# Optimization experiments

Hardware: AMD Instinct MI355X
Metric: run time of the kernel (lower is better)

The kernel has to match this reference:

```python
import jax, jax.numpy as jnp
import numpy as np

ALPHA = 0.2  # leaky relu slope
NEG_BIG = -9000000000000000.0


def setup_inputs() -> dict:
    key = jax.random.key(0)
    k1, k2, k3, k4 = jax.random.split(key, 4)
    B, N, Fin, Fout = 8, 2048, 256, 256
    h = jax.random.normal(k1, (B, N, Fin), dtype=jnp.float32)
    adj = jax.random.randint(k2, (B, N, N), 0, 2, dtype=jnp.int32)
    # xavier_uniform with gain=1.414
    gain = 1.414
    limW = gain * np.sqrt(6.0 / (Fin + Fout))
    W = jax.random.uniform(k3, (Fin, Fout), dtype=jnp.float32, minval=-limW, maxval=limW)
    lima = gain * np.sqrt(6.0 / (2 * Fout + 1))
    a = jax.random.uniform(k4, (2 * Fout, 1), dtype=jnp.float32, minval=-lima, maxval=lima)
    return {"h": h, "adj": adj, "W": W, "a": a}


def reference(h, adj, W, a):
    # Wh: [B, N, F]
    Wh = jnp.matmul(h, W)
    Fout = W.shape[1]
    a1 = a[:Fout, 0]   # scores for source node i (repeat_interleave side)
    a2 = a[Fout:, 0]   # scores for target node j (repeat side)
    # e[b,i,j] = leakyrelu(Wh[b,i]@a1 + Wh[b,j]@a2)  -- decomposed, no O(N^2 * 2F) tensor
    s1 = jnp.einsum('bnf,f->bn', Wh, a1)  # [B, N]
    s2 = jnp.einsum('bnf,f->bn', Wh, a2)  # [B, N]
    e = jax.nn.leaky_relu(s1[:, :, None] + s2[:, None, :], negative_slope=ALPHA)
    masked = jnp.where(adj > 0, e, jnp.full_like(e, NEG_BIG))
    attention = jax.nn.softmax(masked, axis=2)  # dropout=0 (eval mode)
    h_prime = jnp.matmul(attention, Wh)  # [B, N, F]
    return jax.nn.elu(h_prime)
```

## Files before the change

### kernel.cpp

```cpp
#include <hip/hip_runtime.h>

typedef __attribute__((ext_vector_type(8))) short bhalf8;
typedef __attribute__((ext_vector_type(4))) float floatx4;

#define ALPHA_LR 0.2f

__device__ __forceinline__ unsigned short f2bf(float f) {
  union { float f; unsigned int u; } v; v.f = f;
  unsigned int r = v.u + 0x7fffu + ((v.u >> 16) & 1u);
  return (unsigned short)(r >> 16);
}
__device__ __forceinline__ float bf2f(unsigned short u) {
  union { unsigned int u; float f; } v; v.u = ((unsigned int)u) << 16;
  return v.f;
}
__device__ __forceinline__ void gld16(const void* g, void* l) {
  __builtin_amdgcn_global_load_lds((const __attribute__((address_space(1))) unsigned int*)g,
                                   (__attribute__((address_space(3))) unsigned int*)l,
                                   16, 0, 0);
}

__global__ void k0w_split(const float* __restrict__ W,
                          unsigned short* __restrict__ WThi,
                          unsigned short* __restrict__ WTlo,
                          unsigned int* __restrict__ s2maxEnc) {
  __shared__ float s[16][17];
  const int tx = threadIdx.x, ty = threadIdx.y;
  if (blockIdx.x == 0 && blockIdx.y == 0 && ty == 0 && tx < 8) s2maxEnc[tx] = 0u;
  const int n0 = blockIdx.x * 16, k0 = blockIdx.y * 16;
  s[ty][tx] = W[(k0 + ty) * 256 + n0 + tx];
  __syncthreads();
  float v = s[tx][ty];
  const int k = k0 + tx, n = n0 + ty;
  unsigned short hi = f2bf(v);
  unsigned short lo = f2bf(v - bf2f(hi));
  const int idx = (k >> 5) * 8192 + n * 32 + (k & 31);
  WThi[idx] = hi;
  WTlo[idx] = lo;
}

__global__ __launch_bounds__(256) void k2_pack(const int* __restrict__ adj,
                                               unsigned long long* __restrict__ mask) {
  const int wave = threadIdx.x >> 6, lane = threadIdx.x & 63;
  const long wid = (long)blockIdx.x * 4 + wave;
  const long u0 = wid * 64;
  const int* base = adj + u0 * 64 + lane;
#pragma unroll
  for (int it = 0; it < 64; it += 4) {
    int v0 = base[(it + 0) * 64];
    int v1 = base[(it + 1) * 64];
    int v2 = base[(it + 2) * 64];
    int v3 = base[(it + 3) * 64];
    unsigned long long m0 = __ballot(v0 > 0);
    unsigned long long m1 = __ballot(v1 > 0);
    unsigned long long m2 = __ballot(v2 > 0);
    unsigned long long m3 = __ballot(v3 > 0);
    if (lane == 0) {
      mask[u0 + it + 0] = m0;
      mask[u0 + it + 1] = m1;
      mask[u0 + it + 2] = m2;
      mask[u0 + it + 3] = m3;
    }
  }
}

__global__ __launch_bounds__(512, 2) void k1_mfma(const float* __restrict__ h,
                                                  const unsigned short* __restrict__ Bhi_g,
                                                  const unsigned short* __restrict__ Blo_g,
                                                  const float* __restrict__ a_g,
                                                  unsigned short* __restrict__ WhPack,
                                                  float* __restrict__ s1,
                                                  float* __restrict__ s2,
                                                  unsigned int* __restrict__ s2maxEnc) {
  __shared__ unsigned short Ah[64 * 264], Al[64 * 264];
  __shared__ unsigned short Bh[2][8192], Bl[2][8192];
  __shared__ float s1red[64], s2red[64];
  const int t = threadIdx.x;
  const long r0 = (long)blockIdx.x * 64;
  const int wave = t >> 6, lane = t & 63;

  if (t < 64) { s1red[t] = 0.f; s2red[t] = 0.f; }

#pragma unroll
  for (int rep = 0; rep < 2; rep++) {
    const int off = wave * 1024 + rep * 512;
    gld16(Bhi_g + off + lane * 8, &Bh[0][off]);
    gld16(Blo_g + off + lane * 8, &Bl[0][off]);
  }

#pragma unroll
  for (int q = 0; q < 8; q++) {
    int idx = q * 512 + t;
    int row = idx >> 6, c4 = idx & 63;
    float4 x = *(const float4*)(h + (r0 + row) * 256 + c4 * 4);
    float xs[4] = {x.x, x.y, x.z, x.w};
    unsigned short hs[4], ls[4];
#pragma unroll
    for (int qq = 0; qq < 4; qq++) {
      hs[qq] = f2bf(xs[qq]);
      ls[qq] = f2bf(xs[qq] - bf2f(hs[qq]));
    }
    *(ushort4*)&Ah[row * 264 + c4 * 4] = (ushort4){hs[0], hs[1], hs[2], hs[3]};
    *(ushort4*)&Al[row * 264 + c4 * 4] = (ushort4){ls[0], ls[1], ls[2], ls[3]};
  }
  __syncthreads();

  const int wm = wave >> 2, wn = wave & 3;
  const int lhi = lane >> 4, llo = lane & 15;

  floatx4 acc[2][4];
#pragma unroll
  for (int mt = 0; mt < 2; mt++)
#pragma unroll
    for (int nt = 0; nt < 4; nt++) acc[mt][nt] = (floatx4){0.f, 0.f, 0.f, 0.f};

  for (int ks = 0; ks < 8; ks++) {
    const int cur = ks & 1, nxt = cur ^ 1, ksn = (ks + 1) & 7;
#pragma unroll
    for (int rep = 0; rep < 2; rep++) {
      const int off = wave * 1024 + rep * 512;
      gld16(Bhi_g + ksn * 8192 + off + lane * 8, &Bh[nxt][off]);
      gld16(Blo_g + ksn * 8192 + off + lane * 8, &Bl[nxt][off]);
    }

    const int k0 = ks * 32;
    bhalf8 ah[2], al[2], bh[4], bl[4];
#pragma unroll
    for (int mt = 0; mt < 2; mt++) {
      int ro = (wm * 32 + mt * 16 + llo) * 264 + k0 + lhi * 8;
      ah[mt] = *(const bhalf8*)&Ah[ro];
      al[mt] = *(const bhalf8*)&Al[ro];
    }
#pragma unroll
    for (int nt = 0; nt < 4; nt++) {
      int ro = (wn * 64 + nt * 16 + llo) * 32 + lhi * 8;
      bh[nt] = *(const bhalf8*)&Bh[cur][ro];
      bl[nt] = *(const bhalf8*)&Bl[cur][ro];
    }
#pragma unroll
    for (int mt = 0; mt < 2; mt++)
#pragma unroll
      for (int nt = 0; nt < 4; nt++) {
        acc[mt][nt] = __builtin_amdgcn_mfma_f32_16x16x32_bf16(ah[mt], bh[nt], acc[mt][nt], 0, 0, 0);
        acc[mt][nt] = __builtin_amdgcn_mfma_f32_16x16x32_bf16(ah[mt], bl[nt], acc[mt][nt], 0, 0, 0);
        acc[mt][nt] = __builtin_amdgcn_mfma_f32_16x16x32_bf16(al[mt], bh[nt], acc[mt][nt], 0, 0, 0);
      }
    __syncthreads();
  }

  float a1v[4], a2v[4];
#pragma unroll
  for (int nt = 0; nt < 4; nt++) {
    int f = wn * 64 + nt * 16 + llo;
    a1v[nt] = a_g[f];
    a2v[nt] = a_g[256 + f];
  }

  const int b = (int)(r0 >> 11);
  const int jt_base = (int)((r0 & 2047) >> 5);

#pragma unroll
  for (int mt = 0; mt < 2; mt++) {
    float p1[4], p2[4];
#pragma unroll
    for (int reg = 0; reg < 4; reg++) {
      p1[reg] = acc[mt][0][reg] * a1v[0] + acc[mt][1][reg] * a1v[1] +
                acc[mt][2][reg] * a1v[2] + acc[mt][3][reg] * a1v[3];
      p2[reg] = acc[mt][0][reg] * a2v[0] + acc[mt][1][reg] * a2v[1] +
                acc[mt][2][reg] * a2v[2] + acc[mt][3][reg] * a2v[3];
    }
#pragma unroll
    for (int off = 1; off < 16; off <<= 1) {
#pragma unroll
      for (int reg = 0; reg < 4; reg++) {
        p1[reg] += __shfl_xor(p1[reg], off);
        p2[reg] += __shfl_xor(p2[reg], off);
      }
    }
    if (llo == 0) {
#pragma unroll
      for (int reg = 0; reg < 4; reg++) {
        int il = wm * 32 + mt * 16 + lhi * 4 + reg;
        atomicAdd(&s1red[il], p1[reg]);
        atomicAdd(&s2red[il], p2[reg]);
      }
    }
#pragma unroll
    for (int nt = 0; nt < 4; nt++) {
      int f = wn * 64 + nt * 16 + llo;
      int jt = jt_base + wm;
      ushort4 pk = (ushort4){f2bf(acc[mt][nt][0]), f2bf(acc[mt][nt][1]),
                             f2bf(acc[mt][nt][2]), f2bf(acc[mt][nt][3])};
      *(ushort4*)&WhPack[((long)((b * 64 + jt) * 256 + f)) * 32 + mt * 16 + lhi * 4] = pk;
    }
  }

  __syncthreads();
  if (t < 64) {
    s1[r0 + t] = s1red[t];
    s2[r0 + t] = s2red[t];
    float v = s2red[t];
#pragma unroll
    for (int o = 32; o; o >>= 1) v = fmaxf(v, __shfl_xor(v, o));
    if (t == 0) {
      unsigned int u = __float_as_uint(v);
      unsigned int key = (u & 0x80000000u) ? ~u : (u | 0x80000000u);
      atomicMax(s2maxEnc + b, key);
    }
  }
}

__global__ __launch_bounds__(512, 2) void k3_attn(const unsigned short* __restrict__ WhPack,
                                                  const unsigned int* __restrict__ mask32,
                                                  const float* __restrict__ s1g,
                                                  const float* __restrict__ s2g,
                                                  const unsigned int* __restrict__ s2maxEnc,
                                                  float* __restrict__ out) {
  const int t = threadIdx.x;
  const int lin = blockIdx.x;
  const int b = lin & 7;
  const int ig = lin >> 3;
  const int wave = t >> 6, lane = t & 63;
  const int rg = wave >> 2, fg = wave & 3;
  const int i0 = ig * 64 + rg * 32;
  const long gr0 = (long)b * 2048 + i0;
  const int llo = lane & 15, lhi = lane >> 4;
  const int sh = lhi * 8;

  const unsigned int ek = s2maxEnc[b];
  const float s2max = (ek & 0x80000000u) ? __uint_as_float(ek & 0x7fffffffu)
                                         : __uint_as_float(~ek);
  float s1i[2], Mi[2];
#pragma unroll
  for (int mt = 0; mt < 2; mt++) {
    s1i[mt] = s1g[gr0 + mt * 16 + llo];
    float xm = s1i[mt] + s2max;
    Mi[mt] = fmaxf(xm, ALPHA_LR * xm);
  }

  const float* s2p = s2g + (long)b * 2048 + lhi * 8;
  const unsigned int* mp0 = mask32 + (gr0 + llo) * 64;
  const unsigned int* mp1 = mp0 + 16 * 64;
  const unsigned short* wb =
      WhPack + (long)b * 524288 + (long)((fg * 64 + llo) * 32 + lhi * 8);

  unsigned int cm0 = mp0[0], cm1 = mp1[0];
  float4 s2A = *(const float4*)s2p;
  float4 s2B = *(const float4*)(s2p + 4);
  bhalf8 bF[4];
#pragma unroll
  for (int nt = 0; nt < 4; nt++) bF[nt] = *(const bhalf8*)(wb + nt * 512);

  floatx4 acc[2][4];
#pragma unroll
  for (int mt = 0; mt < 2; mt++)
#pragma unroll
    for (int nt = 0; nt < 4; nt++) acc[mt][nt] = (floatx4){0.f, 0.f, 0.f, 0.f};
  float ls0 = 0.f, ls1 = 0.f;

#pragma unroll 2
  for (int jt = 0; jt < 64; jt++) {
    const int jn = (jt < 63) ? jt + 1 : 63;

    bhalf8 bFn[4];
#pragma unroll
    for (int nt = 0; nt < 4; nt++)
      bFn[nt] = *(const bhalf8*)(wb + (long)jn * 8192 + nt * 512);
    float4 s2nA = *(const float4*)(s2p + jn * 32);
    float4 s2nB = *(const float4*)(s2p + jn * 32 + 4);
    unsigned int nm0 = mp0[jn], nm1 = mp1[jn];

    __builtin_amdgcn_sched_barrier(0);

    bhalf8 pa[2];
#pragma unroll
    for (int mt = 0; mt < 2; mt++) {
      const float s1v = s1i[mt], miv = Mi[mt];
      const unsigned int mb = ((mt ? cm1 : cm0) >> sh) & 0xffu;
      float xs[8] = {s2A.x, s2A.y, s2A.z, s2A.w, s2B.x, s2B.y, s2B.z, s2B.w};
      float e[8];
      float lsm = 0.f;
#pragma unroll
      for (int q = 0; q < 8; q++) {
        float x = s1v + xs[q];
        float lk = fmaxf(x, ALPHA_LR * x);
        float ee = __expf(lk - miv);
        ee = (mb & (1u << q)) ? ee : 0.f;
        lsm += ee;
        e[q] = ee;
      }
      if (mt) ls1 += lsm; else ls0 += lsm;
      union { unsigned int u[4]; bhalf8 v; } pk;
#pragma unroll
      for (int q = 0; q < 4; q++)
        asm("v_cvt_pk_bf16_f32 %0, %1, %2" : "=v"(pk.u[q]) : "v"(e[2 * q]), "v"(e[2 * q + 1]));
      pa[mt] = pk.v;
    }

#pragma unroll
    for (int mt = 0; mt < 2; mt++)
#pragma unroll
      for (int nt = 0; nt < 4; nt++)
        acc[mt][nt] = __builtin_amdgcn_mfma_f32_16x16x32_bf16(mt ? pa[1] : pa[0],
                                                              bF[nt], acc[mt][nt], 0, 0, 0);

    cm0 = nm0; cm1 = nm1;
    s2A = s2nA; s2B = s2nB;
#pragma unroll
    for (int nt = 0; nt < 4; nt++) bF[nt] = bFn[nt];
  }

  ls0 += __shfl_xor(ls0, 16); ls0 += __shfl_xor(ls0, 32);
  ls1 += __shfl_xor(ls1, 16); ls1 += __shfl_xor(ls1, 32);
  float inv0 = 1.f / fmaxf(ls0, 1e-35f);
  float inv1 = 1.f / fmaxf(ls1, 1e-35f);

#pragma unroll
  for (int mt = 0; mt < 2; mt++) {
#pragma unroll
    for (int reg = 0; reg < 4; reg++) {
      const int rloc = lhi * 4 + reg;
      float iv = __shfl(mt ? inv1 : inv0, rloc);
      const long orow = (gr0 + mt * 16 + rloc) * 256 + fg * 64 + llo;
#pragma unroll
      for (int nt = 0; nt < 4; nt++) {
        float v = acc[mt][nt][reg] * iv;
        v = v > 0.f ? v : expm1f(v);
        out[orow + nt * 16] = v;
      }
    }
  }
}

extern "C" void kernel_launch(void* const* d_in, const int* in_sizes, int n_in,
                              void* d_out, int out_size, void* d_ws, size_t ws_size,
                              hipStream_t stream) {
  const float* h = (const float*)d_in[0];
  const int* adj = (const int*)d_in[1];
  const float* W = (const float*)d_in[2];
  const float* a = (const float*)d_in[3];
  float* out = (float*)d_out;

  char* ws = (char*)d_ws;
  unsigned short* WhPack = (unsigned short*)ws;
  unsigned short* WThi = (unsigned short*)(ws + 8388608);
  unsigned short* WTlo = (unsigned short*)(ws + 8519680);
  float* s1 = (float*)(ws + 8650752);
  float* s2 = (float*)(ws + 8716288);
  unsigned int* s2maxEnc = (unsigned int*)(ws + 8781824);
  unsigned long long* adjMask = (unsigned long long*)(ws + 8912896);

  hipLaunchKernelGGL(k0w_split, dim3(16, 16), dim3(16, 16), 0, stream, W, WThi, WTlo, s2maxEnc);
  hipLaunchKernelGGL(k1_mfma, dim3(256), dim3(512), 0, stream, h, WThi, WTlo, a,
                     WhPack, s1, s2, s2maxEnc);
  hipLaunchKernelGGL(k2_pack, dim3(2048), dim3(256), 0, stream, adj, adjMask);
  hipLaunchKernelGGL(k3_attn, dim3(256), dim3(512), 0, stream, WhPack,
                     (const unsigned int*)adjMask, s1, s2, s2maxEnc, out);
}
```

Measured before the change: 297.1 us.

## Compute attention probabilities once per block via shared-memory tile, double-buffered

The attention kernel now uses 32-row blocks of 256 threads, launched as twice as many blocks. Each thread computes the exp scores for 4 columns of one row and writes them as bf16 into a double-buffered shared-memory P tile. Each wave then reads its MFMA A operand from that tile and covers 128 output features with 8 accumulators. This removes the redundant per-wave recomputation of exps across feature groups, at the cost of an LDS barrier every iteration and more registers per thread. Wh B-fragments are no longer prefetched a step ahead, and the row sums are reduced through shared memory.

```diff
diff --git a/kernel.cpp b/kernel.cpp
--- a/kernel.cpp
+++ b/kernel.cpp
@@ -210,7 +210,7 @@
   }
 }
 
-__global__ __launch_bounds__(512, 2) void k3_attn(const unsigned short* __restrict__ WhPack,
+__global__ __launch_bounds__(256, 2) void k3_attn(const unsigned short* __restrict__ WhPack,
                                                   const unsigned int* __restrict__ mask32,
                                                   const float* __restrict__ s1g,
                                                   const float* __restrict__ s2g,
@@ -220,114 +220,116 @@
   const int lin = blockIdx.x;
   const int b = lin & 7;
   const int ig = lin >> 3;
+  const int i0 = ig * 32;
+  const long gr0 = (long)b * 2048 + i0;
+
   const int wave = t >> 6, lane = t & 63;
-  const int rg = wave >> 2, fg = wave & 3;
-  const int i0 = ig * 64 + rg * 32;
-  const long gr0 = (long)b * 2048 + i0;
+  const int rg = wave >> 1, fg = wave & 1;
   const int llo = lane & 15, lhi = lane >> 4;
-  const int sh = lhi * 8;
-
+  const int prow = t >> 3;
+  const int jq = (t & 7) * 4;
+
+  __shared__ unsigned short P[2][32][36];
+  __shared__ float lvv[32];
+
+  const float s1i = s1g[gr0 + prow];
   const unsigned int ek = s2maxEnc[b];
   const float s2max = (ek & 0x80000000u) ? __uint_as_float(ek & 0x7fffffffu)
                                          : __uint_as_float(~ek);
-  float s1i[2], Mi[2];
-#pragma unroll
-  for (int mt = 0; mt < 2; mt++) {
-    s1i[mt] = s1g[gr0 + mt * 16 + llo];
-    float xm = s1i[mt] + s2max;
-    Mi[mt] = fmaxf(xm, ALPHA_LR * xm);
-  }
-
-  const float* s2p = s2g + (long)b * 2048 + lhi * 8;
-  const unsigned int* mp0 = mask32 + (gr0 + llo) * 64;
-  const unsigned int* mp1 = mp0 + 16 * 64;
+  const float xm = s1i + s2max;
+  const float Mi = fmaxf(xm, ALPHA_LR * xm);
+
+  const unsigned int* maskrow = mask32 + (gr0 + prow) * 64;
+  const float* s2p = s2g + (long)b * 2048;
   const unsigned short* wb =
-      WhPack + (long)b * 524288 + (long)((fg * 64 + llo) * 32 + lhi * 8);
-
-  unsigned int cm0 = mp0[0], cm1 = mp1[0];
-  float4 s2A = *(const float4*)s2p;
-  float4 s2B = *(const float4*)(s2p + 4);
-  bhalf8 bF[4];
-#pragma unroll
-  for (int nt = 0; nt < 4; nt++) bF[nt] = *(const bhalf8*)(wb + nt * 512);
-
-  floatx4 acc[2][4];
-#pragma unroll
-  for (int mt = 0; mt < 2; mt++)
-#pragma unroll
-    for (int nt = 0; nt < 4; nt++) acc[mt][nt] = (floatx4){0.f, 0.f, 0.f, 0.f};
-  float ls0 = 0.f, ls1 = 0.f;
+      WhPack + (long)b * 524288 + (long)((fg * 128 + llo) * 32 + lhi * 8);
+
+  float lsum = 0.f;
+
+  {
+    unsigned int m = maskrow[0] >> jq;
+    float4 s2v = *(const float4*)(s2p + jq);
+    float xs[4] = {s2v.x, s2v.y, s2v.z, s2v.w};
+    unsigned int pk[2];
+    float e[4];
+#pragma unroll
+    for (int q = 0; q < 4; q++) {
+      float x = s1i + xs[q];
+      float lk = fmaxf(x, ALPHA_LR * x);
+      float ee = __expf(lk - Mi);
+      ee = (m >> q) & 1u ? ee : 0.f;
+      lsum += ee;
+      e[q] = ee;
+    }
+    asm("v_cvt_pk_bf16_f32 %0, %1, %2" : "=v"(pk[0]) : "v"(e[0]), "v"(e[1]));
+    asm("v_cvt_pk_bf16_f32 %0, %1, %2" : "=v"(pk[1]) : "v"(e[2]), "v"(e[3]));
+    *(uint2*)&P[0][prow][jq] = (uint2){pk[0], pk[1]};
+  }
+  unsigned int cm = maskrow[1];
+  float4 cs2 = *(const float4*)(s2p + 32 + jq);
+  asm volatile("s_waitcnt lgkmcnt(0)\n\ts_barrier" ::: "memory");
+
+  floatx4 acc[8];
+#pragma unroll
+  for (int nt = 0; nt < 8; nt++) acc[nt] = (floatx4){0.f, 0.f, 0.f, 0.f};
 
 #pragma unroll 2
   for (int jt = 0; jt < 64; jt++) {
-    const int jn = (jt < 63) ? jt + 1 : 63;
-
-    bhalf8 bFn[4];
-#pragma unroll
-    for (int nt = 0; nt < 4; nt++)
-      bFn[nt] = *(const bhalf8*)(wb + (long)jn * 8192 + nt * 512);
-    float4 s2nA = *(const float4*)(s2p + jn * 32);
-    float4 s2nB = *(const float4*)(s2p + jn * 32 + 4);
-    unsigned int nm0 = mp0[jn], nm1 = mp1[jn];
-
+    const int cur = jt & 1, nxt = cur ^ 1;
+
+    bhalf8 bF[8];
+#pragma unroll
+    for (int nt = 0; nt < 8; nt++)
+      bF[nt] = *(const bhalf8*)(wb + (long)jt * 8192 + nt * 512);
+    const int jp = (jt < 62) ? jt + 2 : 63;
+    unsigned int nm = maskrow[jp];
+    float4 ns2 = *(const float4*)(s2p + jp * 32 + jq);
     __builtin_amdgcn_sched_barrier(0);
 
-    bhalf8 pa[2];
-#pragma unroll
-    for (int mt = 0; mt < 2; mt++) {
-      const float s1v = s1i[mt], miv = Mi[mt];
-      const unsigned int mb = ((mt ? cm1 : cm0) >> sh) & 0xffu;
-      float xs[8] = {s2A.x, s2A.y, s2A.z, s2A.w, s2B.x, s2B.y, s2B.z, s2B.w};
-      float e[8];
-      float lsm = 0.f;
-#pragma unroll
-      for (int q = 0; q < 8; q++) {
-        float x = s1v + xs[q];
+    if (jt < 63) {
+      unsigned int m = cm >> jq;
+      float xs[4] = {cs2.x, cs2.y, cs2.z, cs2.w};
+      unsigned int pk[2];
+      float e[4];
+#pragma unroll
+      for (int q = 0; q < 4; q++) {
+        float x = s1i + xs[q];
         float lk = fmaxf(x, ALPHA_LR * x);
-        float ee = __expf(lk - miv);
-        ee = (mb & (1u << q)) ? ee : 0.f;
-        lsm += ee;
+        float ee = __expf(lk - Mi);
+        ee = (m >> q) & 1u ? ee : 0.f;
+        lsum += ee;
         e[q] = ee;
       }
-      if (mt) ls1 += lsm; else ls0 += lsm;
-      union { unsigned int u[4]; bhalf8 v; } pk;
-#pragma unroll
-      for (int q = 0; q < 4; q++)
-        asm("v_cvt_pk_bf16_f32 %0, %1, %2" : "=v"(pk.u[q]) : "v"(e[2 * q]), "v"(e[2 * q + 1]));
-      pa[mt] = pk.v;
-    }
-
-#pragma unroll
-    for (int mt = 0; mt < 2; mt++)
-#pragma unroll
-      for (int nt = 0; nt < 4; nt++)
-        acc[mt][nt] = __builtin_amdgcn_mfma_f32_16x16x32_bf16(mt ? pa[1] : pa[0],
-                                                              bF[nt], acc[mt][nt], 0, 0, 0);
-
-    cm0 = nm0; cm1 = nm1;
-    s2A = s2nA; s2B = s2nB;
-#pragma unroll
-    for (int nt = 0; nt < 4; nt++) bF[nt] = bFn[nt];
-  }
-
-  ls0 += __shfl_xor(ls0, 16); ls0 += __shfl_xor(ls0, 32);
-  ls1 += __shfl_xor(ls1, 16); ls1 += __shfl_xor(ls1, 32);
-  float inv0 = 1.f / fmaxf(ls0, 1e-35f);
-  float inv1 = 1.f / fmaxf(ls1, 1e-35f);
-
-#pragma unroll
-  for (int mt = 0; mt < 2; mt++) {
-#pragma unroll
-    for (int reg = 0; reg < 4; reg++) {
-      const int rloc = lhi * 4 + reg;
-      float iv = __shfl(mt ? inv1 : inv0, rloc);
-      const long orow = (gr0 + mt * 16 + rloc) * 256 + fg * 64 + llo;
-#pragma unroll
-      for (int nt = 0; nt < 4; nt++) {
-        float v = acc[mt][nt][reg] * iv;
-        v = v > 0.f ? v : expm1f(v);
-        out[orow + nt * 16] = v;
-      }
+      asm("v_cvt_pk_bf16_f32 %0, %1, %2" : "=v"(pk[0]) : "v"(e[0]), "v"(e[1]));
+      asm("v_cvt_pk_bf16_f32 %0, %1, %2" : "=v"(pk[1]) : "v"(e[2]), "v"(e[3]));
+      *(uint2*)&P[nxt][prow][jq] = (uint2){pk[0], pk[1]};
+    }
+    cm = nm; cs2 = ns2;
+
+    bhalf8 af = *(const bhalf8*)&P[cur][rg * 16 + llo][lhi * 8];
+#pragma unroll
+    for (int nt = 0; nt < 8; nt++)
+      acc[nt] = __builtin_amdgcn_mfma_f32_16x16x32_bf16(af, bF[nt], acc[nt], 0, 0, 0);
+
+    asm volatile("s_waitcnt lgkmcnt(0)\n\ts_barrier" ::: "memory");
+  }
+
+  lsum += __shfl_xor(lsum, 1);
+  lsum += __shfl_xor(lsum, 2);
+  lsum += __shfl_xor(lsum, 4);
+  if ((lane & 7) == 0) lvv[prow] = lsum;
+  __syncthreads();
+
+#pragma unroll
+  for (int reg = 0; reg < 4; reg++) {
+    const int rloc = rg * 16 + lhi * 4 + reg;
+    const float iv = 1.f / fmaxf(lvv[rloc], 1e-35f);
+    const long orow = (gr0 + rloc) * 256 + fg * 128 + llo;
+#pragma unroll
+    for (int nt = 0; nt < 8; nt++) {
+      float v = acc[nt][reg] * iv;
+      v = v > 0.f ? v : expm1f(v);
+      out[orow + nt * 16] = v;
     }
   }
 }
@@ -354,6 +356,6 @@
   hipLaunchKernelGGL(k1_mfma, dim3(256), dim3(512), 0, stream, h, WThi, WTlo, a,
                      WhPack, s1, s2, s2maxEnc);
   hipLaunchKernelGGL(k2_pack, dim3(2048), dim3(256), 0, stream, adj, adjMask);
-  hipLaunchKernelGGL(k3_attn, dim3(256), dim3(512), 0, stream, WhPack,
+  hipLaunchKernelGGL(k3_attn, dim3(512), dim3(256), 0, stream, WhPack,
                      (const unsigned int*)adjMask, s1, s2, s2maxEnc, out);
 }
```

After: 295.2 us. About the same (-0.6%).

## Stage Wh tiles and attention probabilities in LDS with double buffering

Applied to the files above, without the earlier changes.

The attention kernel now loads 64-column Wh tiles into double-buffered shared memory via global_load_lds and stores the s2 vector in LDS. The exp/mask probabilities are computed once per (row, column) by 8 threads per row and written to an LDS P tile. Before, each feature-group wave recomputed them and read Wh fragments straight from global memory. This removes the redundant exp work across the four feature-group waves and shares Wh loads across the block. In exchange it adds a barrier per step and about 110KB of LDS, which may cap occupancy below the requested 2 blocks per CU.

```diff
diff --git a/kernel.cpp b/kernel.cpp
--- a/kernel.cpp
+++ b/kernel.cpp
@@ -220,108 +220,144 @@
   const int lin = blockIdx.x;
   const int b = lin & 7;
   const int ig = lin >> 3;
+  const long gr0 = (long)b * 2048 + ig * 64;
+
   const int wave = t >> 6, lane = t & 63;
   const int rg = wave >> 2, fg = wave & 3;
-  const int i0 = ig * 64 + rg * 32;
-  const long gr0 = (long)b * 2048 + i0;
   const int llo = lane & 15, lhi = lane >> 4;
-  const int sh = lhi * 8;
-
+
+  __shared__ unsigned short WhL[2][16384];
+  __shared__ unsigned short Pl[2][64 * 72];
+  __shared__ float s2l[2048];
+  __shared__ float lvv[64];
+
+  const int pr = t >> 3;
+  const int pq = t & 7;
+  const int q2 = pq >> 2;
+  const int shq = (pq & 3) * 8;
+
+  const float s1i = s1g[gr0 + pr];
   const unsigned int ek = s2maxEnc[b];
   const float s2max = (ek & 0x80000000u) ? __uint_as_float(ek & 0x7fffffffu)
                                          : __uint_as_float(~ek);
-  float s1i[2], Mi[2];
+  const float xm = s1i + s2max;
+  const float Mi = fmaxf(xm, ALPHA_LR * xm);
+  const unsigned int* mrow = mask32 + (gr0 + pr) * 64;
+
+  const int gsrc8 = (((lane & 3) ^ ((lane >> 3) & 3))) * 8;
+  const unsigned short* wsrcB =
+      WhPack + (long)b * 524288 + wave * 512 + (lane >> 2) * 32 + gsrc8;
+
+  const int boff = fg * 2048 + llo * 32 + (lhi ^ ((llo >> 1) & 3)) * 8;
+  const int aoff = (rg * 32 + llo) * 72 + lhi * 8;
+
+  *(float4*)&s2l[t * 4] = *(const float4*)(s2g + (long)b * 2048 + t * 4);
+#pragma unroll
+  for (int i = 0; i < 4; i++)
+    gld16(wsrcB + i * 4096, &WhL[0][i * 4096 + wave * 512]);
+  unsigned int m0 = mrow[q2];
+  __syncthreads();
+
+  float lsum = 0.f;
+  {
+    unsigned int mb = m0 >> shq;
+    float4 sA = *(const float4*)&s2l[pq * 8];
+    float4 sB = *(const float4*)&s2l[pq * 8 + 4];
+    float xs[8] = {sA.x, sA.y, sA.z, sA.w, sB.x, sB.y, sB.z, sB.w};
+    unsigned int pk[4];
+    float e[8];
+#pragma unroll
+    for (int q = 0; q < 8; q++) {
+      float x = s1i + xs[q];
+      float lk = fmaxf(x, ALPHA_LR * x);
+      float ee = __expf(lk - Mi);
+      ee = (mb >> q) & 1u ? ee : 0.f;
+      lsum += ee;
+      e[q] = ee;
+    }
+#pragma unroll
+    for (int q = 0; q < 4; q++)
+      asm("v_cvt_pk_bf16_f32 %0, %1, %2" : "=v"(pk[q]) : "v"(e[2 * q]), "v"(e[2 * q + 1]));
+    *(uint4*)&Pl[0][pr * 72 + pq * 8] = (uint4){pk[0], pk[1], pk[2], pk[3]};
+  }
+  unsigned int mC = mrow[2 + q2];
+  __syncthreads();
+
+  floatx4 acc[2][4];
+#pragma unroll
+  for (int mt = 0; mt < 2; mt++)
+#pragma unroll
+    for (int nt = 0; nt < 4; nt++) acc[mt][nt] = (floatx4){0.f, 0.f, 0.f, 0.f};
+
+#pragma unroll 2
+  for (int step = 0; step < 32; step++) {
+    const int cur = step & 1, nxt = cur ^ 1;
+
+    if (step < 31) {
+      const long jb = (long)(step + 1) * 16384;
+#pragma unroll
+      for (int i = 0; i < 4; i++)
+        gld16(wsrcB + jb + i * 4096, &WhL[nxt][i * 4096 + wave * 512]);
+    }
+    unsigned int mN = mrow[(step < 30 ? (step + 2) * 2 : 62) + q2];
+    __builtin_amdgcn_sched_barrier(0);
+
+    if (step < 31) {
+      unsigned int mb = mC >> shq;
+      const int sbase = (step + 1) * 64 + pq * 8;
+      float4 sA = *(const float4*)&s2l[sbase];
+      float4 sB = *(const float4*)&s2l[sbase + 4];
+      float xs[8] = {sA.x, sA.y, sA.z, sA.w, sB.x, sB.y, sB.z, sB.w};
+      unsigned int pk[4];
+      float e[8];
+#pragma unroll
+      for (int q = 0; q < 8; q++) {
+        float x = s1i + xs[q];
+        float lk = fmaxf(x, ALPHA_LR * x);
+        float ee = __expf(lk - Mi);
+        ee = (mb >> q) & 1u ? ee : 0.f;
+        lsum += ee;
+        e[q] = ee;
+      }
+#pragma unroll
+      for (int q = 0; q < 4; q++)
+        asm("v_cvt_pk_bf16_f32 %0, %1, %2" : "=v"(pk[q]) : "v"(e[2 * q]), "v"(e[2 * q + 1]));
+      *(uint4*)&Pl[nxt][pr * 72 + pq * 8] = (uint4){pk[0], pk[1], pk[2], pk[3]};
+    }
+    mC = mN;
+
+#pragma unroll
+    for (int kk = 0; kk < 2; kk++) {
+      bhalf8 aF[2], bF[4];
+#pragma unroll
+      for (int mt = 0; mt < 2; mt++)
+        aF[mt] = *(const bhalf8*)&Pl[cur][aoff + mt * 1152 + kk * 32];
+#pragma unroll
+      for (int nt = 0; nt < 4; nt++)
+        bF[nt] = *(const bhalf8*)&WhL[cur][kk * 8192 + nt * 512 + boff];
+#pragma unroll
+      for (int mt = 0; mt < 2; mt++)
+#pragma unroll
+        for (int nt = 0; nt < 4; nt++)
+          acc[mt][nt] = __builtin_amdgcn_mfma_f32_16x16x32_bf16(aF[mt], bF[nt], acc[mt][nt], 0, 0, 0);
+    }
+
+    __syncthreads();
+  }
+
+  lsum += __shfl_xor(lsum, 1);
+  lsum += __shfl_xor(lsum, 2);
+  lsum += __shfl_xor(lsum, 4);
+  if ((lane & 7) == 0) lvv[pr] = lsum;
+  __syncthreads();
+
 #pragma unroll
   for (int mt = 0; mt < 2; mt++) {
-    s1i[mt] = s1g[gr0 + mt * 16 + llo];
-    float xm = s1i[mt] + s2max;
-    Mi[mt] = fmaxf(xm, ALPHA_LR * xm);
-  }
-
-  const float* s2p = s2g + (long)b * 2048 + lhi * 8;
-  const unsigned int* mp0 = mask32 + (gr0 + llo) * 64;
-  const unsigned int* mp1 = mp0 + 16 * 64;
-  const unsigned short* wb =
-      WhPack + (long)b * 524288 + (long)((fg * 64 + llo) * 32 + lhi * 8);
-
-  unsigned int cm0 = mp0[0], cm1 = mp1[0];
-  float4 s2A = *(const float4*)s2p;
-  float4 s2B = *(const float4*)(s2p + 4);
-  bhalf8 bF[4];
-#pragma unroll
-  for (int nt = 0; nt < 4; nt++) bF[nt] = *(const bhalf8*)(wb + nt * 512);
-
-  floatx4 acc[2][4];
-#pragma unroll
-  for (int mt = 0; mt < 2; mt++)
-#pragma unroll
-    for (int nt = 0; nt < 4; nt++) acc[mt][nt] = (floatx4){0.f, 0.f, 0.f, 0.f};
-  float ls0 = 0.f, ls1 = 0.f;
-
-#pragma unroll 2
-  for (int jt = 0; jt < 64; jt++) {
-    const int jn = (jt < 63) ? jt + 1 : 63;
-
-    bhalf8 bFn[4];
-#pragma unroll
-    for (int nt = 0; nt < 4; nt++)
-      bFn[nt] = *(const bhalf8*)(wb + (long)jn * 8192 + nt * 512);
-    float4 s2nA = *(const float4*)(s2p + jn * 32);
-    float4 s2nB = *(const float4*)(s2p + jn * 32 + 4);
-    unsigned int nm0 = mp0[jn], nm1 = mp1[jn];
-
-    __builtin_amdgcn_sched_barrier(0);
-
-    bhalf8 pa[2];
-#pragma unroll
-    for (int mt = 0; mt < 2; mt++) {
-      const float s1v = s1i[mt], miv = Mi[mt];
-      const unsigned int mb = ((mt ? cm1 : cm0) >> sh) & 0xffu;
-      float xs[8] = {s2A.x, s2A.y, s2A.z, s2A.w, s2B.x, s2B.y, s2B.z, s2B.w};
-      float e[8];
-      float lsm = 0.f;
-#pragma unroll
-      for (int q = 0; q < 8; q++) {
-        float x = s1v + xs[q];
-        float lk = fmaxf(x, ALPHA_LR * x);
-        float ee = __expf(lk - miv);
-        ee = (mb & (1u << q)) ? ee : 0.f;
-        lsm += ee;
-        e[q] = ee;
-      }
-      if (mt) ls1 += lsm; else ls0 += lsm;
-      union { unsigned int u[4]; bhalf8 v; } pk;
-#pragma unroll
-      for (int q = 0; q < 4; q++)
-        asm("v_cvt_pk_bf16_f32 %0, %1, %2" : "=v"(pk.u[q]) : "v"(e[2 * q]), "v"(e[2 * q + 1]));
-      pa[mt] = pk.v;
-    }
-
-#pragma unroll
-    for (int mt = 0; mt < 2; mt++)
-#pragma unroll
-      for (int nt = 0; nt < 4; nt++)
-        acc[mt][nt] = __builtin_amdgcn_mfma_f32_16x16x32_bf16(mt ? pa[1] : pa[0],
-                                                              bF[nt], acc[mt][nt], 0, 0, 0);
-
-    cm0 = nm0; cm1 = nm1;
-    s2A = s2nA; s2B = s2nB;
-#pragma unroll
-    for (int nt = 0; nt < 4; nt++) bF[nt] = bFn[nt];
-  }
-
-  ls0 += __shfl_xor(ls0, 16); ls0 += __shfl_xor(ls0, 32);
-  ls1 += __shfl_xor(ls1, 16); ls1 += __shfl_xor(ls1, 32);
-  float inv0 = 1.f / fmaxf(ls0, 1e-35f);
-  float inv1 = 1.f / fmaxf(ls1, 1e-35f);
-
-#pragma unroll
-  for (int mt = 0; mt < 2; mt++) {
 #pragma unroll
     for (int reg = 0; reg < 4; reg++) {
-      const int rloc = lhi * 4 + reg;
-      float iv = __shfl(mt ? inv1 : inv0, rloc);
-      const long orow = (gr0 + mt * 16 + rloc) * 256 + fg * 64 + llo;
+      const int rloc = rg * 32 + mt * 16 + lhi * 4 + reg;
+      const float iv = 1.f / fmaxf(lvv[rloc], 1e-35f);
+      const long orow = (gr0 + rloc) * 256 + fg * 64 + llo;
 #pragma unroll
       for (int nt = 0; nt < 4; nt++) {
         float v = acc[mt][nt][reg] * iv;
```

New measurement: 264.9 us. 10.8% less time.
